# Performance work log

Hardware: AMD Instinct MI355X
Metric: run time of the kernel (lower is better)

Reference implementation:

```python
import jax, jax.numpy as jnp
import numpy as np

N_NODES = 100000
N_EDGES = 1600000
IN_FEATS, N_HIDDEN, N_CLASSES = 128, 64, 40


def setup_inputs() -> dict:
    key = jax.random.key(0)
    ks = jax.random.split(key, 6)
    h = jax.random.normal(ks[0], (N_NODES, IN_FEATS), dtype=jnp.float32)
    W0 = jax.random.normal(ks[1], (IN_FEATS, N_HIDDEN), dtype=jnp.float32) * (1.0 / np.sqrt(IN_FEATS))
    b0 = jnp.zeros((N_HIDDEN,), dtype=jnp.float32)
    W1 = jax.random.normal(ks[2], (N_HIDDEN, N_HIDDEN), dtype=jnp.float32) * (1.0 / np.sqrt(N_HIDDEN))
    b1 = jnp.zeros((N_HIDDEN,), dtype=jnp.float32)
    W2 = jax.random.normal(ks[3], (N_HIDDEN, N_CLASSES), dtype=jnp.float32) * (1.0 / np.sqrt(N_HIDDEN))
    b2 = jnp.zeros((N_CLASSES,), dtype=jnp.float32)
    src = jax.random.randint(ks[4], (N_EDGES,), 0, N_NODES, dtype=jnp.int32)
    dst = jax.random.randint(ks[5], (N_EDGES,), 0, N_NODES, dtype=jnp.int32)
    return {"h": h, "W0": W0, "b0": b0, "W1": W1, "b1": b1, "W2": W2, "b2": b2, "src": src, "dst": dst}


def _degrees(src, dst):
    ones = jnp.ones(src.shape[0], dtype=jnp.float32)
    out_deg = jax.ops.segment_sum(ones, src, num_segments=N_NODES)
    in_deg = jax.ops.segment_sum(ones, dst, num_segments=N_NODES)
    # DGL clamps degrees to >= 1 (allow_zero_in_degree)
    norm_src = jax.lax.rsqrt(jnp.maximum(out_deg, 1.0))  # [N]
    norm_dst = jax.lax.rsqrt(jnp.maximum(in_deg, 1.0))   # [N]
    return norm_src, norm_dst


def _graph_conv(x, W, b, src, dst, norm_src, norm_dst, act):
    # DGL GraphConv, norm='both': D_in^{-1/2} A^T D_out^{-1/2} (X W) + b
    xw = (x @ W) * norm_src[:, None]               # [N, out]
    agg = jax.ops.segment_sum(xw[src], dst, num_segments=N_NODES)  # gather-scatter over edges
    out = agg * norm_dst[:, None] + b
    return jax.nn.relu(out) if act else out


def reference(h, W0, b0, W1, b1, W2, b2, src, dst):
    norm_src, norm_dst = _degrees(src, dst)
    h = _graph_conv(h, W0, b0, src, dst, norm_src, norm_dst, act=True)
    # dropout layers are identity at inference
    h = _graph_conv(h, W1, b1, src, dst, norm_src, norm_dst, act=True)
    h = _graph_conv(h, W2, b2, src, dst, norm_src, norm_dst, act=False)
    return h
```

## Files before the change

### kernel.cpp

```cpp
#include <hip/hip_runtime.h>
#include <hip/hip_fp16.h>

#define N_NODES 100000
#define N_EDGES 1600000
#define ELL_W 64
#define NCHUNK 32
#define NSEG 8
#define CH (N_EDGES / NCHUNK)
#define SEGN (N_NODES / NSEG)

typedef unsigned short ushort4v __attribute__((ext_vector_type(4)));
typedef _Float16 half8 __attribute__((ext_vector_type(8)));
typedef float floatx4 __attribute__((ext_vector_type(4)));


__global__ __launch_bounds__(512) void k_count(const int* __restrict__ src, const int* __restrict__ dst,
                                               unsigned char* __restrict__ cnt_out,
                                               unsigned char* __restrict__ cnt_in) {
    __shared__ int ci[SEGN];
    __shared__ int co[SEGN];
    const int c = blockIdx.x;
    const int lo = blockIdx.y * SEGN;
    for (int i = threadIdx.x; i < SEGN; i += 512) { ci[i] = 0; co[i] = 0; }
    __syncthreads();
    const int4* s4 = (const int4*)(src + c * CH);
    const int4* d4 = (const int4*)(dst + c * CH);
    for (int i = threadIdx.x; i < CH / 4; i += 512) {
        int4 s = s4[i], d = d4[i];
        unsigned a;
        a = (unsigned)(s.x - lo); if (a < SEGN) atomicAdd(&co[a], 1);
        a = (unsigned)(s.y - lo); if (a < SEGN) atomicAdd(&co[a], 1);
        a = (unsigned)(s.z - lo); if (a < SEGN) atomicAdd(&co[a], 1);
        a = (unsigned)(s.w - lo); if (a < SEGN) atomicAdd(&co[a], 1);
        a = (unsigned)(d.x - lo); if (a < SEGN) atomicAdd(&ci[a], 1);
        a = (unsigned)(d.y - lo); if (a < SEGN) atomicAdd(&ci[a], 1);
        a = (unsigned)(d.z - lo); if (a < SEGN) atomicAdd(&ci[a], 1);
        a = (unsigned)(d.w - lo); if (a < SEGN) atomicAdd(&ci[a], 1);
    }
    __syncthreads();
    for (int i = threadIdx.x; i < SEGN; i += 512) {
        cnt_in [c * N_NODES + lo + i] = (unsigned char)ci[i];
        cnt_out[c * N_NODES + lo + i] = (unsigned char)co[i];
    }
}

__global__ __launch_bounds__(256) void k_scan(unsigned char* __restrict__ cnt_in,
                                              const unsigned char* __restrict__ cnt_out,
                                              int* __restrict__ fill, float* __restrict__ norm_src,
                                              float* __restrict__ norm_dst) {
    int d = blockIdx.x * 256 + threadIdx.x;
    if (d >= N_NODES) return;
    int run = 0;
    #pragma unroll
    for (int c = 0; c < NCHUNK; ++c) {
        int v = cnt_in[c * N_NODES + d];
        cnt_in[c * N_NODES + d] = (unsigned char)run;
        run += v;
    }
    int od = 0;
    #pragma unroll
    for (int c = 0; c < NCHUNK; ++c) od += cnt_out[c * N_NODES + d];
    fill[d] = run;
    norm_dst[d] = rsqrtf((float)(run < 1 ? 1 : run));
    norm_src[d] = rsqrtf((float)(od  < 1 ? 1 : od ));
}

__global__ __launch_bounds__(512) void k_scatter(const int* __restrict__ src, const int* __restrict__ dst,
                                                 const unsigned char* __restrict__ bases,
                                                 int* __restrict__ ell) {
    __shared__ int base[SEGN];
    const int c = blockIdx.x;
    const int lo = blockIdx.y * SEGN;
    for (int i = threadIdx.x; i < SEGN; i += 512) base[i] = bases[c * N_NODES + lo + i];
    __syncthreads();
    const int4* s4 = (const int4*)(src + c * CH);
    const int4* d4 = (const int4*)(dst + c * CH);
    for (int i = threadIdx.x; i < CH / 4; i += 512) {
        int4 s = s4[i], d = d4[i];
        unsigned r; int p;
        r = (unsigned)(d.x - lo); if (r < SEGN) { p = atomicAdd(&base[r], 1); if (p < ELL_W) ell[p * N_NODES + lo + r] = s.x; }
        r = (unsigned)(d.y - lo); if (r < SEGN) { p = atomicAdd(&base[r], 1); if (p < ELL_W) ell[p * N_NODES + lo + r] = s.y; }
        r = (unsigned)(d.z - lo); if (r < SEGN) { p = atomicAdd(&base[r], 1); if (p < ELL_W) ell[p * N_NODES + lo + r] = s.z; }
        r = (unsigned)(d.w - lo); if (r < SEGN) { p = atomicAdd(&base[r], 1); if (p < ELL_W) ell[p * N_NODES + lo + r] = s.w; }
    }
}

template<int K, int NCOL>
__global__ __launch_bounds__(256) void k_gemm(const float* __restrict__ Xv, const float* __restrict__ W,
                                              const float* __restrict__ norm, __half* __restrict__ Y) {
    constexpr int NT = (NCOL + 15) / 16;
    constexpr int NR = NT * 16;
    __shared__ __align__(16) _Float16 Xh[64][K + 8];
    __shared__ __align__(16) _Float16 Wt[NR][K + 8];
    const int tid = threadIdx.x;
    const int row0 = blockIdx.x * 64;

    for (int idx = tid; idx < K * NCOL; idx += 256) {
        int k = idx / NCOL, c = idx - (idx / NCOL) * NCOL;
        Wt[c][k] = (_Float16)W[idx];
    }
    for (int idx = tid; idx < (NR - NCOL) * K; idx += 256) {
        int c = NCOL + idx / K, k = idx - (idx / K) * K;
        Wt[c][k] = (_Float16)0;
    }

    for (int idx = tid; idx < 64 * (K / 8); idx += 256) {
        int r = idx / (K / 8), kc = idx - (idx / (K / 8)) * (K / 8);
        int gr = row0 + r;
        half8 v = {0, 0, 0, 0, 0, 0, 0, 0};
        if (gr < N_NODES) {
            const float* X = Xv + (long)gr * K + kc * 8;
            float4 u0 = *(const float4*)(X + 0);
            float4 u1 = *(const float4*)(X + 4);
            v.s0 = (_Float16)u0.x; v.s1 = (_Float16)u0.y;
            v.s2 = (_Float16)u0.z; v.s3 = (_Float16)u0.w;
            v.s4 = (_Float16)u1.x; v.s5 = (_Float16)u1.y;
            v.s6 = (_Float16)u1.z; v.s7 = (_Float16)u1.w;
        }
        *(half8*)&Xh[r][kc * 8] = v;
    }
    __syncthreads();

    const int lane = tid & 63;
    const int wave = tid >> 6;
    const int quad = lane >> 4;
    const int l16 = lane & 15;
    const int r0 = wave * 16;

    floatx4 acc[NT] = {};
    #pragma unroll
    for (int k0 = 0; k0 < K; k0 += 32) {
        half8 a = *(const half8*)&Xh[r0 + l16][k0 + quad * 8];
        #pragma unroll
        for (int t = 0; t < NT; ++t) {
            half8 b = *(const half8*)&Wt[t * 16 + l16][k0 + quad * 8];
            acc[t] = __builtin_amdgcn_mfma_f32_16x16x32_f16(a, b, acc[t], 0, 0, 0);
        }
    }

    #pragma unroll
    for (int i = 0; i < 4; ++i) {
        int gr = row0 + r0 + quad * 4 + i;
        if (gr < N_NODES) {
            float s = norm[gr];
            #pragma unroll
            for (int t = 0; t < NT; ++t) {
                int c = t * 16 + l16;
                if (c < NCOL) Y[(long)gr * NCOL + c] = __float2half(acc[t][i] * s);
            }
        }
    }
}

template<int K, int NCOL>
__global__ __launch_bounds__(256) void k_agg_gemm(const __half* __restrict__ XWp, const int* __restrict__ ell,
                                                  const int* __restrict__ deg, const float* __restrict__ norm_dst,
                                                  const float* __restrict__ biasp, const float* __restrict__ W,
                                                  const float* __restrict__ norm, __half* __restrict__ Y) {
    constexpr int NT = (NCOL + 15) / 16;
    constexpr int NR = NT * 16;
    constexpr int NQ = K / 8;
    __shared__ __align__(16) _Float16 Xh[64][K + 8];
    __shared__ __align__(16) _Float16 Wt[NR][K + 8];
    const int tid = threadIdx.x;
    const int row0 = blockIdx.x * 64;

    for (int idx = tid; idx < K * NCOL; idx += 256) {
        int k = idx / NCOL, c = idx - (idx / NCOL) * NCOL;
        Wt[c][k] = (_Float16)W[idx];
    }
    for (int idx = tid; idx < (NR - NCOL) * K; idx += 256) {
        int c = NCOL + idx / K, k = idx - (idx / K) * K;
        Wt[c][k] = (_Float16)0;
    }

    for (int item = tid; item < 64 * NQ; item += 256) {
        int r = item / NQ, q = item - (item / NQ) * NQ;
        int d = row0 + r;
        _Float16 res[8] = {};
        if (d < N_NODES) {
            int dg = deg[d]; if (dg > ELL_W) dg = ELL_W;
            float acc[8] = {};
            int j = 0;
            for (; j + 4 <= dg; j += 4) {
                int i0 = __builtin_nontemporal_load(ell + (j + 0) * N_NODES + d);
                int i1 = __builtin_nontemporal_load(ell + (j + 1) * N_NODES + d);
                int i2 = __builtin_nontemporal_load(ell + (j + 2) * N_NODES + d);
                int i3 = __builtin_nontemporal_load(ell + (j + 3) * N_NODES + d);
                float4 r0v = *(const float4*)(XWp + (long)i0 * K + q * 8);
                float4 r1v = *(const float4*)(XWp + (long)i1 * K + q * 8);
                float4 r2v = *(const float4*)(XWp + (long)i2 * K + q * 8);
                float4 r3v = *(const float4*)(XWp + (long)i3 * K + q * 8);
                const __half2* h0 = (const __half2*)&r0v;
                const __half2* h1 = (const __half2*)&r1v;
                const __half2* h2 = (const __half2*)&r2v;
                const __half2* h3 = (const __half2*)&r3v;
                #pragma unroll
                for (int t = 0; t < 4; ++t) {
                    float2 f0 = __half22float2(h0[t]);
                    float2 f1 = __half22float2(h1[t]);
                    float2 f2 = __half22float2(h2[t]);
                    float2 f3 = __half22float2(h3[t]);
                    acc[2 * t + 0] += (f0.x + f1.x) + (f2.x + f3.x);
                    acc[2 * t + 1] += (f0.y + f1.y) + (f2.y + f3.y);
                }
            }
            for (; j < dg; ++j) {
                int s = __builtin_nontemporal_load(ell + j * N_NODES + d);
                float4 rv = *(const float4*)(XWp + (long)s * K + q * 8);
                const __half2* hh = (const __half2*)&rv;
                #pragma unroll
                for (int t = 0; t < 4; ++t) {
                    float2 f = __half22float2(hh[t]);
                    acc[2 * t + 0] += f.x;
                    acc[2 * t + 1] += f.y;
                }
            }
            float nd = norm_dst[d];
            #pragma unroll
            for (int t = 0; t < 8; ++t) {
                float o = acc[t] * nd + biasp[q * 8 + t];
                res[t] = (_Float16)fmaxf(o, 0.f);
            }
        }
        *(half8*)&Xh[r][q * 8] = *(const half8*)res;
    }
    __syncthreads();

    const int lane = tid & 63;
    const int wave = tid >> 6;
    const int quad = lane >> 4;
    const int l16 = lane & 15;
    const int r0 = wave * 16;

    floatx4 acc[NT] = {};
    #pragma unroll
    for (int k0 = 0; k0 < K; k0 += 32) {
        half8 a = *(const half8*)&Xh[r0 + l16][k0 + quad * 8];
        #pragma unroll
        for (int t = 0; t < NT; ++t) {
            half8 b = *(const half8*)&Wt[t * 16 + l16][k0 + quad * 8];
            acc[t] = __builtin_amdgcn_mfma_f32_16x16x32_f16(a, b, acc[t], 0, 0, 0);
        }
    }

    #pragma unroll
    for (int i = 0; i < 4; ++i) {
        int gr = row0 + r0 + quad * 4 + i;
        if (gr < N_NODES) {
            float s = norm[gr];
            #pragma unroll
            for (int t = 0; t < NT; ++t) {
                int c = t * 16 + l16;
                if (c < NCOL) Y[(long)gr * NCOL + c] = __float2half(acc[t][i] * s);
            }
        }
    }
}

template<int NF>
__global__ __launch_bounds__(256) void k_agg(const __half* __restrict__ XW, const int* __restrict__ ell,
                                             const int* __restrict__ deg, const float* __restrict__ norm_dst,
                                             const float* __restrict__ bias, float* __restrict__ OUT) {
    constexpr int NQ = NF / 8;
    int gid = blockIdx.x * 256 + threadIdx.x;
    int d = gid / NQ;
    int q = gid - d * NQ;
    if (d >= N_NODES) return;
    int dg = deg[d]; if (dg > ELL_W) dg = ELL_W;

    float acc[8] = {};
    int j = 0;
    for (; j + 4 <= dg; j += 4) {
        int i0 = __builtin_nontemporal_load(ell + (j + 0) * N_NODES + d);
        int i1 = __builtin_nontemporal_load(ell + (j + 1) * N_NODES + d);
        int i2 = __builtin_nontemporal_load(ell + (j + 2) * N_NODES + d);
        int i3 = __builtin_nontemporal_load(ell + (j + 3) * N_NODES + d);
        float4 r0 = *(const float4*)(XW + (long)i0 * NF + q * 8);
        float4 r1 = *(const float4*)(XW + (long)i1 * NF + q * 8);
        float4 r2 = *(const float4*)(XW + (long)i2 * NF + q * 8);
        float4 r3 = *(const float4*)(XW + (long)i3 * NF + q * 8);
        const __half2* h0 = (const __half2*)&r0;
        const __half2* h1 = (const __half2*)&r1;
        const __half2* h2 = (const __half2*)&r2;
        const __half2* h3 = (const __half2*)&r3;
        #pragma unroll
        for (int t = 0; t < 4; ++t) {
            float2 f0 = __half22float2(h0[t]);
            float2 f1 = __half22float2(h1[t]);
            float2 f2 = __half22float2(h2[t]);
            float2 f3 = __half22float2(h3[t]);
            acc[2 * t + 0] += (f0.x + f1.x) + (f2.x + f3.x);
            acc[2 * t + 1] += (f0.y + f1.y) + (f2.y + f3.y);
        }
    }
    for (; j < dg; ++j) {
        int s = __builtin_nontemporal_load(ell + j * N_NODES + d);
        float4 r = *(const float4*)(XW + (long)s * NF + q * 8);
        const __half2* hh = (const __half2*)&r;
        #pragma unroll
        for (int t = 0; t < 4; ++t) {
            float2 f = __half22float2(hh[t]);
            acc[2 * t + 0] += f.x;
            acc[2 * t + 1] += f.y;
        }
    }

    float nd = norm_dst[d];
    float o[8];
    #pragma unroll
    for (int t = 0; t < 8; ++t) o[t] = acc[t] * nd + bias[q * 8 + t];
    *(float4*)(OUT + (long)d * NF + q * 8 + 0) = make_float4(o[0], o[1], o[2], o[3]);
    *(float4*)(OUT + (long)d * NF + q * 8 + 4) = make_float4(o[4], o[5], o[6], o[7]);
}

extern "C" void kernel_launch(void* const* d_in, const int* in_sizes, int n_in,
                              void* d_out, int out_size, void* d_ws, size_t ws_size,
                              hipStream_t stream) {
    const float* h  = (const float*)d_in[0];
    const float* W0 = (const float*)d_in[1];
    const float* b0 = (const float*)d_in[2];
    const float* W1 = (const float*)d_in[3];
    const float* b1 = (const float*)d_in[4];
    const float* W2 = (const float*)d_in[5];
    const float* b2 = (const float*)d_in[6];
    const int* src  = (const int*)d_in[7];
    const int* dst  = (const int*)d_in[8];
    float* out = (float*)d_out;

    char* ws = (char*)d_ws;
    size_t off = 0;
    int* fill        = (int*)(ws + off); off += (size_t)N_NODES * 4;
    float* norm_src  = (float*)(ws + off); off += (size_t)N_NODES * 4;
    float* norm_dst  = (float*)(ws + off); off += (size_t)N_NODES * 4;
    int* ell         = (int*)(ws + off); off += (size_t)N_NODES * ELL_W * 4;
    unsigned char* cnt_in  = (unsigned char*)(ws + off); off += (size_t)NCHUNK * N_NODES;
    unsigned char* cnt_out = (unsigned char*)(ws + off); off += (size_t)NCHUNK * N_NODES;
    __half* bufA  = (__half*)(ws + off); off += (size_t)N_NODES * 64 * 2;
    __half* bufB  = (__half*)(ws + off); off += (size_t)N_NODES * 64 * 2;

    k_count<<<dim3(NCHUNK, NSEG), 512, 0, stream>>>(src, dst, cnt_out, cnt_in);
    k_scan<<<(N_NODES + 255) / 256, 256, 0, stream>>>(cnt_in, cnt_out, fill, norm_src, norm_dst);
    k_scatter<<<dim3(NCHUNK, NSEG), 512, 0, stream>>>(src, dst, cnt_in, ell);

    const int grid = (N_NODES + 63) / 64;

    k_gemm<128, 64><<<grid, 256, 0, stream>>>(h, W0, norm_src, bufA);
    k_agg_gemm<64, 64><<<grid, 256, 0, stream>>>(bufA, ell, fill, norm_dst, b0, W1, norm_src, bufB);
    k_agg_gemm<64, 40><<<grid, 256, 0, stream>>>(bufB, ell, fill, norm_dst, b1, W2, norm_src, bufA);
    k_agg<40><<<(N_NODES * 5 + 255) / 256, 256, 0, stream>>>(bufA, ell, fill, norm_dst, b2, out);
}
```

Before: 284.2 us.

## Stage ELL neighbor indices in shared memory and deepen gather unrolling

Each 64-row block now loads its rows' ELL neighbor indices cooperatively into shared memory (up to the block's max degree) before aggregation. Previously every feature-quarter thread reloaded the same index from global memory. The gather loop is unrolled to 8 outstanding row loads for more memory-level parallelism. The final aggregation kernel is restructured into 64-node blocks of 320 threads to share the same staging. The cost is extra LDS use (about 17KB for indices), two block barriers, and index loads bounded by the block's max degree.

```diff
diff --git a/kernel.cpp b/kernel.cpp
--- a/kernel.cpp
+++ b/kernel.cpp
@@ -9,7 +9,6 @@
 #define CH (N_EDGES / NCHUNK)
 #define SEGN (N_NODES / NSEG)
 
-typedef unsigned short ushort4v __attribute__((ext_vector_type(4)));
 typedef _Float16 half8 __attribute__((ext_vector_type(8)));
 typedef float floatx4 __attribute__((ext_vector_type(4)));
 
@@ -162,6 +161,9 @@
     constexpr int NQ = K / 8;
     __shared__ __align__(16) _Float16 Xh[64][K + 8];
     __shared__ __align__(16) _Float16 Wt[NR][K + 8];
+    __shared__ int sIdx[64][65];
+    __shared__ int sDeg[64];
+    __shared__ int sMax;
     const int tid = threadIdx.x;
     const int row0 = blockIdx.x * 64;
 
@@ -174,41 +176,40 @@
         Wt[c][k] = (_Float16)0;
     }
 
+    if (tid < 64) {
+        int node = row0 + tid;
+        int dg = 0;
+        if (node < N_NODES) { dg = deg[node]; if (dg > ELL_W) dg = ELL_W; }
+        sDeg[tid] = dg;
+        int v = dg;
+        #pragma unroll
+        for (int o = 32; o > 0; o >>= 1) v = max(v, __shfl_down(v, o));
+        if (tid == 0) sMax = v;
+    }
+    __syncthreads();
+    const int mdeg = sMax;
+    for (int i = tid; i < mdeg * 64; i += 256) {
+        int slot = i >> 6, r = i & 63;
+        int node = row0 + r;
+        sIdx[r][slot] = (node < N_NODES) ? ell[slot * N_NODES + node] : 0;
+    }
+    __syncthreads();
+
     for (int item = tid; item < 64 * NQ; item += 256) {
         int r = item / NQ, q = item - (item / NQ) * NQ;
         int d = row0 + r;
-        _Float16 res[8] = {};
-        if (d < N_NODES) {
-            int dg = deg[d]; if (dg > ELL_W) dg = ELL_W;
-            float acc[8] = {};
-            int j = 0;
-            for (; j + 4 <= dg; j += 4) {
-                int i0 = __builtin_nontemporal_load(ell + (j + 0) * N_NODES + d);
-                int i1 = __builtin_nontemporal_load(ell + (j + 1) * N_NODES + d);
-                int i2 = __builtin_nontemporal_load(ell + (j + 2) * N_NODES + d);
-                int i3 = __builtin_nontemporal_load(ell + (j + 3) * N_NODES + d);
-                float4 r0v = *(const float4*)(XWp + (long)i0 * K + q * 8);
-                float4 r1v = *(const float4*)(XWp + (long)i1 * K + q * 8);
-                float4 r2v = *(const float4*)(XWp + (long)i2 * K + q * 8);
-                float4 r3v = *(const float4*)(XWp + (long)i3 * K + q * 8);
-                const __half2* h0 = (const __half2*)&r0v;
-                const __half2* h1 = (const __half2*)&r1v;
-                const __half2* h2 = (const __half2*)&r2v;
-                const __half2* h3 = (const __half2*)&r3v;
-                #pragma unroll
-                for (int t = 0; t < 4; ++t) {
-                    float2 f0 = __half22float2(h0[t]);
-                    float2 f1 = __half22float2(h1[t]);
-                    float2 f2 = __half22float2(h2[t]);
-                    float2 f3 = __half22float2(h3[t]);
-                    acc[2 * t + 0] += (f0.x + f1.x) + (f2.x + f3.x);
-                    acc[2 * t + 1] += (f0.y + f1.y) + (f2.y + f3.y);
-                }
-            }
-            for (; j < dg; ++j) {
-                int s = __builtin_nontemporal_load(ell + j * N_NODES + d);
-                float4 rv = *(const float4*)(XWp + (long)s * K + q * 8);
-                const __half2* hh = (const __half2*)&rv;
+        int dg = sDeg[r];
+        const int* idxr = sIdx[r];
+        float acc[8] = {};
+        int j = 0;
+        for (; j + 8 <= dg; j += 8) {
+            float4 v[8];
+            #pragma unroll
+            for (int u = 0; u < 8; ++u)
+                v[u] = *(const float4*)(XWp + (long)idxr[j + u] * K + q * 8);
+            #pragma unroll
+            for (int u = 0; u < 8; ++u) {
+                const __half2* hh = (const __half2*)&v[u];
                 #pragma unroll
                 for (int t = 0; t < 4; ++t) {
                     float2 f = __half22float2(hh[t]);
@@ -216,6 +217,19 @@
                     acc[2 * t + 1] += f.y;
                 }
             }
+        }
+        for (; j < dg; ++j) {
+            float4 rv = *(const float4*)(XWp + (long)idxr[j] * K + q * 8);
+            const __half2* hh = (const __half2*)&rv;
+            #pragma unroll
+            for (int t = 0; t < 4; ++t) {
+                float2 f = __half22float2(hh[t]);
+                acc[2 * t + 0] += f.x;
+                acc[2 * t + 1] += f.y;
+            }
+        }
+        _Float16 res[8] = {};
+        if (d < N_NODES) {
             float nd = norm_dst[d];
             #pragma unroll
             for (int t = 0; t < 8; ++t) {
@@ -259,45 +273,62 @@
 }
 
 template<int NF>
-__global__ __launch_bounds__(256) void k_agg(const __half* __restrict__ XW, const int* __restrict__ ell,
-                                             const int* __restrict__ deg, const float* __restrict__ norm_dst,
-                                             const float* __restrict__ bias, float* __restrict__ OUT) {
+__global__ __launch_bounds__(320) void k_agg_f(const __half* __restrict__ XW, const int* __restrict__ ell,
+                                               const int* __restrict__ deg, const float* __restrict__ norm_dst,
+                                               const float* __restrict__ bias, float* __restrict__ OUT) {
     constexpr int NQ = NF / 8;
-    int gid = blockIdx.x * 256 + threadIdx.x;
-    int d = gid / NQ;
-    int q = gid - d * NQ;
+    __shared__ int sIdx[64][65];
+    __shared__ int sDeg[64];
+    __shared__ int sMax;
+    const int tid = threadIdx.x;
+    const int row0 = blockIdx.x * 64;
+
+    if (tid < 64) {
+        int node = row0 + tid;
+        int dg = 0;
+        if (node < N_NODES) { dg = deg[node]; if (dg > ELL_W) dg = ELL_W; }
+        sDeg[tid] = dg;
+        int v = dg;
+        #pragma unroll
+        for (int o = 32; o > 0; o >>= 1) v = max(v, __shfl_down(v, o));
+        if (tid == 0) sMax = v;
+    }
+    __syncthreads();
+    const int mdeg = sMax;
+    for (int i = tid; i < mdeg * 64; i += 320) {
+        int slot = i >> 6, r = i & 63;
+        int node = row0 + r;
+        sIdx[r][slot] = (node < N_NODES) ? ell[slot * N_NODES + node] : 0;
+    }
+    __syncthreads();
+
+    const int r = tid / NQ, q = tid - (tid / NQ) * NQ;
+    const int d = row0 + r;
     if (d >= N_NODES) return;
-    int dg = deg[d]; if (dg > ELL_W) dg = ELL_W;
+    const int dg = sDeg[r];
+    const int* idxr = sIdx[r];
 
     float acc[8] = {};
     int j = 0;
-    for (; j + 4 <= dg; j += 4) {
-        int i0 = __builtin_nontemporal_load(ell + (j + 0) * N_NODES + d);
-        int i1 = __builtin_nontemporal_load(ell + (j + 1) * N_NODES + d);
-        int i2 = __builtin_nontemporal_load(ell + (j + 2) * N_NODES + d);
-        int i3 = __builtin_nontemporal_load(ell + (j + 3) * N_NODES + d);
-        float4 r0 = *(const float4*)(XW + (long)i0 * NF + q * 8);
-        float4 r1 = *(const float4*)(XW + (long)i1 * NF + q * 8);
-        float4 r2 = *(const float4*)(XW + (long)i2 * NF + q * 8);
-        float4 r3 = *(const float4*)(XW + (long)i3 * NF + q * 8);
-        const __half2* h0 = (const __half2*)&r0;
-        const __half2* h1 = (const __half2*)&r1;
-        const __half2* h2 = (const __half2*)&r2;
-        const __half2* h3 = (const __half2*)&r3;
-        #pragma unroll
-        for (int t = 0; t < 4; ++t) {
-            float2 f0 = __half22float2(h0[t]);
-            float2 f1 = __half22float2(h1[t]);
-            float2 f2 = __half22float2(h2[t]);
-            float2 f3 = __half22float2(h3[t]);
-            acc[2 * t + 0] += (f0.x + f1.x) + (f2.x + f3.x);
-            acc[2 * t + 1] += (f0.y + f1.y) + (f2.y + f3.y);
+    for (; j + 8 <= dg; j += 8) {
+        float4 v[8];
+        #pragma unroll
+        for (int u = 0; u < 8; ++u)
+            v[u] = *(const float4*)(XW + (long)idxr[j + u] * NF + q * 8);
+        #pragma unroll
+        for (int u = 0; u < 8; ++u) {
+            const __half2* hh = (const __half2*)&v[u];
+            #pragma unroll
+            for (int t = 0; t < 4; ++t) {
+                float2 f = __half22float2(hh[t]);
+                acc[2 * t + 0] += f.x;
+                acc[2 * t + 1] += f.y;
+            }
         }
     }
     for (; j < dg; ++j) {
-        int s = __builtin_nontemporal_load(ell + j * N_NODES + d);
-        float4 r = *(const float4*)(XW + (long)s * NF + q * 8);
-        const __half2* hh = (const __half2*)&r;
+        float4 rv = *(const float4*)(XW + (long)idxr[j] * NF + q * 8);
+        const __half2* hh = (const __half2*)&rv;
         #pragma unroll
         for (int t = 0; t < 4; ++t) {
             float2 f = __half22float2(hh[t]);
@@ -348,5 +379,5 @@
     k_gemm<128, 64><<<grid, 256, 0, stream>>>(h, W0, norm_src, bufA);
     k_agg_gemm<64, 64><<<grid, 256, 0, stream>>>(bufA, ell, fill, norm_dst, b0, W1, norm_src, bufB);
     k_agg_gemm<64, 40><<<grid, 256, 0, stream>>>(bufB, ell, fill, norm_dst, b1, W2, norm_src, bufA);
-    k_agg<40><<<(N_NODES * 5 + 255) / 256, 256, 0, stream>>>(bufA, ell, fill, norm_dst, b2, out);
-}
+    k_agg_f<40><<<grid, 320, 0, stream>>>(bufA, ell, fill, norm_dst, b2, out);
+}
```

After: 275.9 us. 1.03x faster.
